# Performance work log

Hardware: AMD Instinct MI355X
Metric: run time of the kernel (lower is better)

## Reference

```python
import jax, jax.numpy as jnp
import numpy as np

N = 100000   # nodes / embedding vocab
E = 1600000  # edges
D = 128      # feature dim
R = 7        # num relations
B = 4096     # matches
EPS = 1e-5


def setup_inputs() -> dict:
    key = jax.random.key(0)
    ks = jax.random.split(key, 12)
    s = 0.05
    return {
        "x": jnp.arange(N, dtype=jnp.int32),
        "edge_index": jax.random.randint(ks[0], (2, E), 0, N, dtype=jnp.int32),
        "edge_type": jax.random.randint(ks[1], (E,), 0, R, dtype=jnp.int32),
        "home": jax.random.randint(ks[2], (B,), 0, N, dtype=jnp.int32),
        "away": jax.random.randint(ks[3], (B,), 0, N, dtype=jnp.int32),
        "embed": jax.random.normal(ks[4], (N, D), jnp.float32) * s,
        "rel_w": jax.random.normal(ks[5], (3, R, D, D), jnp.float32) * s,
        "root_w": jax.random.normal(ks[6], (3, D, D), jnp.float32) * s,
        "conv_b": jnp.zeros((3, D), jnp.float32),
        "bn_gamma": jnp.ones((2, D), jnp.float32),
        "bn_beta": jnp.zeros((2, D), jnp.float32),
        "bn_mean": jnp.zeros((2, D), jnp.float32),
        "bn_var": jnp.ones((2, D), jnp.float32),
        "fc0_w": jax.random.normal(ks[7], (256, 2 * D), jnp.float32) * s,
        "fc0_b": jnp.zeros((256,), jnp.float32),
        "fc1_w": jax.random.normal(ks[8], (128, 256), jnp.float32) * s,
        "fc1_b": jnp.zeros((128,), jnp.float32),
        "fc2_w": jax.random.normal(ks[9], (3, 128), jnp.float32) * s,
        "fc2_b": jnp.zeros((3,), jnp.float32),
    }


def rgcn_conv(h, rel_w, root_w, bias, src, dst, seg):
    # PyG RGCNConv with aggr='mean': per-relation mean of source features,
    # aggregate-then-transform (valid since the relation transform is linear).
    n = h.shape[0]
    agg = jax.ops.segment_sum(h[src], seg, num_segments=n * R)      # [N*R, Din]
    cnt = jax.ops.segment_sum(jnp.ones((src.shape[0],), h.dtype), seg,
                              num_segments=n * R)                   # [N*R]
    agg = (agg / jnp.maximum(cnt, 1.0)[:, None]).reshape(n, R, -1)  # [N, R, Din]
    return jnp.einsum('nri,rio->no', agg, rel_w) + h @ root_w + bias


def reference(x, edge_index, edge_type, home, away, embed, rel_w, root_w, conv_b,
              bn_gamma, bn_beta, bn_mean, bn_var,
              fc0_w, fc0_b, fc1_w, fc1_b, fc2_w, fc2_b):
    src, dst = edge_index[0], edge_index[1]
    seg = dst.astype(jnp.int32) * R + edge_type  # combined (node, relation) id

    h = embed[x]  # [N, D]
    for l in range(2):
        h = rgcn_conv(h, rel_w[l], root_w[l], conv_b[l], src, dst, seg)
        h = (h - bn_mean[l]) * jax.lax.rsqrt(bn_var[l] + EPS) * bn_gamma[l] + bn_beta[l]
        h = jax.nn.relu(h)
    h = rgcn_conv(h, rel_w[2], root_w[2], conv_b[2], src, dst, seg)

    g = jnp.concatenate([h[home], h[away]], axis=1)  # [B, 2D]
    g = jax.nn.relu(g @ fc0_w.T + fc0_b)
    g = jax.nn.relu(g @ fc1_w.T + fc1_b)
    g = g @ fc2_w.T + fc2_b
    return jax.nn.log_softmax(g, axis=1)
```

## Files before the change

### kernel.cpp

```cpp
#include <hip/hip_runtime.h>
#include <hip/hip_bf16.h>

#define RR 7
#define EPSBN 1e-5f

typedef __attribute__((ext_vector_type(8))) __bf16 bf16x8;
typedef __attribute__((ext_vector_type(4))) float f32x4;
typedef __attribute__((ext_vector_type(2))) float f32x2;

__device__ __forceinline__ float uhi2f(unsigned int u) {
    union { unsigned int i; float f; } c; c.i = u; return c.f;
}
__device__ __forceinline__ unsigned short f2b(float f) {
    union { float f; unsigned int i; } c; c.f = f;
    unsigned int x = c.i;
    return (unsigned short)((x + 0x7fffu + ((x >> 16) & 1u)) >> 16);
}

__global__ void hist_k(const int* __restrict__ dst, const int* __restrict__ et,
                       int* __restrict__ cnt, int ne) {
    int e = blockIdx.x * 256 + threadIdx.x;
    if (e < ne) atomicAdd(&cnt[dst[e] * RR + et[e]], 1);
}
__global__ void scan1_k(const int* __restrict__ cnt, int* __restrict__ bsum, int n) {
    __shared__ int sh[256];
    int base = blockIdx.x << 10;
    int s = 0;
    for (int i = threadIdx.x; i < 1024; i += 256) { int idx = base + i; if (idx < n) s += cnt[idx]; }
    sh[threadIdx.x] = s; __syncthreads();
    for (int off = 128; off > 0; off >>= 1) {
        if (threadIdx.x < off) sh[threadIdx.x] += sh[threadIdx.x + off];
        __syncthreads();
    }
    if (threadIdx.x == 0) bsum[blockIdx.x] = sh[0];
}
__global__ void scan2_k(int* __restrict__ bsum, int nb) {
    __shared__ int sh[256];
    int t = threadIdx.x;
    int v[4]; int loc = 0;
#pragma unroll
    for (int i = 0; i < 4; ++i) { int idx = t * 4 + i; v[i] = (idx < nb) ? bsum[idx] : 0; loc += v[i]; }
    sh[t] = loc; __syncthreads();
    for (int off = 1; off < 256; off <<= 1) {
        int x = (t >= off) ? sh[t - off] : 0;
        __syncthreads();
        sh[t] += x;
        __syncthreads();
    }
    int ex = (t > 0) ? sh[t - 1] : 0;
#pragma unroll
    for (int i = 0; i < 4; ++i) { int idx = t * 4 + i; if (idx < nb) { int vv = v[i]; bsum[idx] = ex; ex += vv; } }
}
__global__ void scan3_k(const int* __restrict__ cnt, const int* __restrict__ boff,
                        int* __restrict__ ptr, int* __restrict__ cursor, int n, int total) {
    __shared__ int sh[256];
    int t = threadIdx.x;
    int base = (blockIdx.x << 10) + (t << 2);
    int v[4]; int loc = 0;
#pragma unroll
    for (int i = 0; i < 4; ++i) { int idx = base + i; v[i] = (idx < n) ? cnt[idx] : 0; loc += v[i]; }
    sh[t] = loc; __syncthreads();
    for (int off = 1; off < 256; off <<= 1) {
        int x = (t >= off) ? sh[t - off] : 0;
        __syncthreads();
        sh[t] += x;
        __syncthreads();
    }
    int ex = boff[blockIdx.x] + ((t > 0) ? sh[t - 1] : 0);
#pragma unroll
    for (int i = 0; i < 4; ++i) {
        int idx = base + i;
        if (idx < n) { ptr[idx] = ex; cursor[idx] = ex; ex += v[i]; }
    }
    if (blockIdx.x == 0 && t == 0) ptr[n] = total;
}
__global__ void scatter_k(const int* __restrict__ src, const int* __restrict__ dst,
                          const int* __restrict__ et, int* __restrict__ cursor,
                          int* __restrict__ ssorted, int ne) {
    int e = blockIdx.x * 256 + threadIdx.x;
    if (e < ne) {
        int seg = dst[e] * RR + et[e];
        int pos = atomicAdd(&cursor[seg], 1);
        ssorted[pos] = src[e];
    }
}

__global__ __launch_bounds__(256) void prep_w_k(const float* __restrict__ rel_w,
                                                const float* __restrict__ root_w,
                                                unsigned short* __restrict__ wall) {
    __shared__ unsigned short T[128][130];
    int l = blockIdx.x >> 3, kb = blockIdx.x & 7;
    const float* src = (kb < RR) ? rel_w + ((size_t)(l * RR + kb) << 14)
                                 : root_w + ((size_t)l << 14);
    int t = threadIdx.x;
    for (int c = t; c < 4096; c += 256) {
        float4 f = *(const float4*)(src + (c << 2));
        int i = c >> 5, o = (c & 31) << 2;
        T[i][o] = f2b(f.x); T[i][o+1] = f2b(f.y); T[i][o+2] = f2b(f.z); T[i][o+3] = f2b(f.w);
    }
    __syncthreads();
    unsigned short* dst = wall + ((size_t)blockIdx.x << 14);
    for (int c = t; c < 2048; c += 256) {
        int frag = c >> 6;
        int lane = c & 63;
        int ks = frag >> 3, nt = frag & 7;
        int o = (nt << 4) + (lane & 15);
        int ib = (ks << 5) + ((lane >> 4) << 3);
        uint4 o4;
        o4.x = (unsigned)T[ib+0][o] | ((unsigned)T[ib+1][o] << 16);
        o4.y = (unsigned)T[ib+2][o] | ((unsigned)T[ib+3][o] << 16);
        o4.z = (unsigned)T[ib+4][o] | ((unsigned)T[ib+5][o] << 16);
        o4.w = (unsigned)T[ib+6][o] | ((unsigned)T[ib+7][o] << 16);
        *(uint4*)(dst + (c << 3)) = o4;
    }
}
__global__ void prep_h_k(const int* __restrict__ x, const float* __restrict__ embed,
                         unsigned short* __restrict__ h, int n) {
    int i = blockIdx.x * 256 + threadIdx.x;
    if (i >= n * 16) return;
    int node = i >> 4, c8 = (i & 15) << 3;
    const float* e = embed + ((size_t)x[node] << 7) + c8;
    float4 f0 = *(const float4*)e;
    float4 f1 = *(const float4*)(e + 4);
    uint4 o4;
    o4.x = (unsigned)f2b(f0.x) | ((unsigned)f2b(f0.y) << 16);
    o4.y = (unsigned)f2b(f0.z) | ((unsigned)f2b(f0.w) << 16);
    o4.z = (unsigned)f2b(f1.x) | ((unsigned)f2b(f1.y) << 16);
    o4.w = (unsigned)f2b(f1.z) | ((unsigned)f2b(f1.w) << 16);
    *(uint4*)(h + ((size_t)node << 7) + c8) = o4;
}
__global__ void prep_misc_k(const float* __restrict__ fc0w, const float* __restrict__ fc1w,
                            float* __restrict__ w0t, float* __restrict__ w1t,
                            const float* __restrict__ conv_b,
                            const float* __restrict__ bn_g, const float* __restrict__ bn_b,
                            const float* __restrict__ bn_m, const float* __restrict__ bn_v,
                            float* __restrict__ AB) {
    int b = blockIdx.x;
    if (b < 256) {
        int idx = (b << 8) + threadIdx.x;
        int o = idx & 255, i = idx >> 8;
        w0t[idx] = fc0w[o * 256 + i];
    } else if (b < 384) {
        int idx = ((b - 256) << 8) + threadIdx.x;
        int o = idx & 127, i = idx >> 7;
        w1t[idx] = fc1w[o * 256 + i];
    } else {
        for (int t = threadIdx.x; t < 384; t += 256) {
            int l = t >> 7, j = t & 127;
            float A = 1.f, Bv = conv_b[(l << 7) + j];
            if (l < 2) {
                float sc = bn_g[(l << 7) + j] * rsqrtf(bn_v[(l << 7) + j] + EPSBN);
                A = sc;
                Bv = Bv * sc + (bn_b[(l << 7) + j] - bn_m[(l << 7) + j] * sc);
            }
            AB[(l << 8) + j] = A;
            AB[(l << 8) + 128 + j] = Bv;
        }
    }
}

#define PAIRF(w) ((f32x2){uhi2f((w) << 16), uhi2f((w) & 0xffff0000u)})
#define ACCP(b, u) { av2[(b)+0] += PAIRF((u).x); av2[(b)+1] += PAIRF((u).y); \
                     av2[(b)+2] += PAIRF((u).z); av2[(b)+3] += PAIRF((u).w); }
#define GATH(s) { const unsigned short* hp = h_in + ((size_t)(s) << 7) + (quad << 3); \
                  uint4 u0 = *(const uint4*)(hp);       uint4 u1 = *(const uint4*)(hp + 32); \
                  uint4 u2 = *(const uint4*)(hp + 64);  uint4 u3 = *(const uint4*)(hp + 96); \
                  ACCP(0, u0); ACCP(4, u1); ACCP(8, u2); ACCP(12, u3); }

__global__ __launch_bounds__(256, 4) void layer_k(
    const unsigned short* __restrict__ h_in,
    unsigned short* __restrict__ h_out,
    const unsigned short* __restrict__ wfrag,
    const float* __restrict__ AB,
    const int* __restrict__ seg_ptr, const int* __restrict__ src_sorted,
    const int* __restrict__ list_a, const int* __restrict__ list_b, int listB,
    int nout, int bnrelu)
{
    const int tid  = threadIdx.x;
    const int wave = tid >> 6;
    const int lane = tid & 63;
    const int n16  = lane & 15;
    const int quad = lane >> 4;
    const int row0 = blockIdx.x << 6;
    const int gidx = row0 + (wave << 4) + n16;
    const bool valid = gidx < nout;
    int gnode = 0;
    if (valid) {
        gnode = list_a ? (gidx < listB ? list_a[gidx] : list_b[gidx - listB]) : gidx;
    }

    int p[8];
    {
        int b = valid ? gnode * RR : 0;
#pragma unroll
        for (int i = 0; i < 8; ++i) p[i] = seg_ptr[b + i];
    }

    f32x4 acc[8];
#pragma unroll
    for (int i = 0; i < 8; ++i) acc[i] = (f32x4){0.f, 0.f, 0.f, 0.f};

    int sv0, sv1, sv2, sv3;
    { int e0 = p[0]; sv0 = src_sorted[e0]; sv1 = src_sorted[e0+1];
      sv2 = src_sorted[e0+2]; sv3 = src_sorted[e0+3]; }

    const unsigned short* wl = wfrag + (lane << 3);

#pragma unroll
    for (int kb = 0; kb < 8; ++kb) {
        f32x2 av2[16];
#pragma unroll
        for (int i = 0; i < 16; ++i) av2[i] = (f32x2){0.f, 0.f};
        float scale = 1.f;
        int nv0 = 0, nv1 = 0, nv2 = 0, nv3 = 0;
        if (kb < RR) {
            if (kb < RR - 1) {
                int en = p[kb + 1];
                nv0 = src_sorted[en]; nv1 = src_sorted[en+1];
                nv2 = src_sorted[en+2]; nv3 = src_sorted[en+3];
            }
            if (valid) {
                int e0 = p[kb], e1 = p[kb + 1];
                int cnt = e1 - e0;
                if (cnt > 0) scale = __builtin_amdgcn_rcpf((float)cnt);
                if (cnt > 0) GATH(sv0);
                if (cnt > 1) GATH(sv1);
                if (cnt > 2) GATH(sv2);
                if (cnt > 3) GATH(sv3);
                for (int e = e0 + 4; e < e1; ++e) {
                    int s = src_sorted[e];
                    GATH(s);
                }
            }
        } else {
            if (valid) GATH(gnode);
        }
        uint4 au[4];
#pragma unroll
        for (int ks = 0; ks < 4; ++ks) {
            unsigned pw[4];
#pragma unroll
            for (int m = 0; m < 4; ++m) {
                f32x2 q = av2[(ks << 2) + m] * scale;
                __hip_bfloat162 b2 = __float22bfloat162_rn(make_float2(q.x, q.y));
                unsigned u; __builtin_memcpy(&u, &b2, 4);
                pw[m] = u;
            }
            au[ks].x = pw[0]; au[ks].y = pw[1]; au[ks].z = pw[2]; au[ks].w = pw[3];
        }
        const unsigned short* wk = wl + (kb << 14);
#pragma unroll
        for (int ks = 0; ks < 4; ++ks) {
            bf16x8 af;
            __builtin_memcpy(&af, &au[ks], 16);
#pragma unroll
            for (int nt = 0; nt < 8; ++nt) {
                bf16x8 bfr = *(const bf16x8*)(wk + (((ks << 3) + nt) << 9));
                acc[nt] = __builtin_amdgcn_mfma_f32_16x16x32_bf16(af, bfr, acc[nt], 0, 0, 0);
            }
        }
        sv0 = nv0; sv1 = nv1; sv2 = nv2; sv3 = nv3;
    }

#pragma unroll
    for (int nt = 0; nt < 8; ++nt) {
        int j = (nt << 4) + n16;
        float Aj = AB[j];
        float Bj = AB[128 + j];
#pragma unroll
        for (int r = 0; r < 4; ++r) {
            int orow = row0 + (wave << 4) + (quad << 2) + r;
            if (orow < nout) {
                float v = acc[nt][r] * Aj + Bj;
                if (bnrelu) v = fmaxf(v, 0.f);
                h_out[((size_t)orow << 7) + j] = f2b(v);
            }
        }
    }
}

__global__ __launch_bounds__(256) void mlp_k(
    const unsigned short* __restrict__ hC,
    const float* __restrict__ w0t, const float* __restrict__ bb0,
    const float* __restrict__ w1t, const float* __restrict__ bb1,
    const float* __restrict__ w2, const float* __restrict__ bb2,
    float* __restrict__ out, int Bn)
{
    __shared__ __attribute__((aligned(16))) float g0[16][256];
    __shared__ __attribute__((aligned(16))) float g1[16][256];
    __shared__ float lg[16][4];
    int t = threadIdx.x;
    {
        int row = t >> 4;
        int cseg = (t & 15) << 4;
        int gr = (blockIdx.x << 4) + row;
        int gc = (gr < Bn) ? gr : 0;
        const unsigned short* sp = (cseg < 128) ? (hC + ((size_t)gc << 7) + cseg)
                                                : (hC + ((size_t)(Bn + gc) << 7) + (cseg - 128));
#pragma unroll
        for (int c8 = 0; c8 < 2; ++c8) {
            uint4 v = *(const uint4*)(sp + (c8 << 3));
            int base = cseg + (c8 << 3);
            g0[row][base+0] = uhi2f(v.x << 16); g0[row][base+1] = uhi2f(v.x & 0xffff0000u);
            g0[row][base+2] = uhi2f(v.y << 16); g0[row][base+3] = uhi2f(v.y & 0xffff0000u);
            g0[row][base+4] = uhi2f(v.z << 16); g0[row][base+5] = uhi2f(v.z & 0xffff0000u);
            g0[row][base+6] = uhi2f(v.w << 16); g0[row][base+7] = uhi2f(v.w & 0xffff0000u);
        }
    }
    __syncthreads();
    {
        float acc[16];
#pragma unroll
        for (int r = 0; r < 16; ++r) acc[r] = 0.f;
#pragma unroll 4
        for (int i = 0; i < 256; ++i) {
            float w = w0t[(i << 8) + t];
#pragma unroll
            for (int r = 0; r < 16; ++r) acc[r] += w * g0[r][i];
        }
        float bb = bb0[t];
#pragma unroll
        for (int r = 0; r < 16; ++r) g1[r][t] = fmaxf(acc[r] + bb, 0.f);
    }
    __syncthreads();
    {
        int o = t & 127, rg = t >> 7;
        float acc[8];
#pragma unroll
        for (int r = 0; r < 8; ++r) acc[r] = 0.f;
#pragma unroll 4
        for (int i = 0; i < 256; ++i) {
            float w = w1t[(i << 7) + o];
#pragma unroll
            for (int r = 0; r < 8; ++r) acc[r] += w * g1[(rg << 3) + r][i];
        }
        float bb = bb1[o];
#pragma unroll
        for (int r = 0; r < 8; ++r) g0[(rg << 3) + r][o] = fmaxf(acc[r] + bb, 0.f);
    }
    __syncthreads();
    if (t < 48) {
        int row = t / 3, cls = t - row * 3;
        const float* wr = w2 + (cls << 7);
        float a = 0.f;
        for (int i = 0; i < 128; i += 4) {
            float4 w = *(const float4*)(wr + i);
            float4 g = *(const float4*)&g0[row][i];
            a += w.x * g.x + w.y * g.y + w.z * g.z + w.w * g.w;
        }
        lg[row][cls] = a + bb2[cls];
    }
    __syncthreads();
    if (t < 16) {
        int gr = (blockIdx.x << 4) + t;
        if (gr < Bn) {
            float l0 = lg[t][0], l1 = lg[t][1], l2 = lg[t][2];
            float m = fmaxf(l0, fmaxf(l1, l2));
            float lse = m + logf(expf(l0 - m) + expf(l1 - m) + expf(l2 - m));
            out[gr * 3 + 0] = l0 - lse;
            out[gr * 3 + 1] = l1 - lse;
            out[gr * 3 + 2] = l2 - lse;
        }
    }
}

extern "C" void kernel_launch(void* const* d_in, const int* in_sizes, int n_in,
                              void* d_out, int out_size, void* d_ws, size_t ws_size,
                              hipStream_t stream) {
    const int*   x      = (const int*)d_in[0];
    const int*   eidx   = (const int*)d_in[1];
    const int*   etype  = (const int*)d_in[2];
    const int*   home   = (const int*)d_in[3];
    const int*   away   = (const int*)d_in[4];
    const float* embed  = (const float*)d_in[5];
    const float* rel_w  = (const float*)d_in[6];
    const float* root_w = (const float*)d_in[7];
    const float* conv_b = (const float*)d_in[8];
    const float* bn_g   = (const float*)d_in[9];
    const float* bn_b   = (const float*)d_in[10];
    const float* bn_m   = (const float*)d_in[11];
    const float* bn_v   = (const float*)d_in[12];
    const float* fc0w   = (const float*)d_in[13];
    const float* fc0b   = (const float*)d_in[14];
    const float* fc1w   = (const float*)d_in[15];
    const float* fc1b   = (const float*)d_in[16];
    const float* fc2w   = (const float*)d_in[17];
    const float* fc2b   = (const float*)d_in[18];
    float* out = (float*)d_out;

    const int N_ = in_sizes[0];
    const int E_ = in_sizes[2];
    const int B_ = in_sizes[3];
    const int NS = N_ * RR;

    char* ws = (char*)d_ws;
    auto alloc = [&](size_t bytes) -> char* {
        char* p = ws;
        ws += (bytes + 255) & ~(size_t)255;
        return p;
    };
    int* ptr         = (int*)alloc((size_t)(NS + 1) * 4);
    int* cursor      = (int*)alloc((size_t)NS * 4);
    int* bsum        = (int*)alloc(4096);
    int* src_sorted  = (int*)alloc((size_t)(E_ + 16) * 4);
    unsigned short* wall = (unsigned short*)alloc((size_t)3 * 8 * 16384 * 2);
    unsigned short* hA   = (unsigned short*)alloc((size_t)N_ * 128 * 2);
    unsigned short* hB   = (unsigned short*)alloc((size_t)N_ * 128 * 2);
    unsigned short* hC   = (unsigned short*)alloc((size_t)2 * B_ * 128 * 2);
    float* AB        = (float*)alloc(3 * 256 * 4);
    float* w0t       = (float*)alloc(65536 * 4);
    float* w1t       = (float*)alloc(32768 * 4);

    const int nb = (NS + 1023) / 1024;

    (void)hipMemsetAsync(cursor, 0, (size_t)NS * 4, stream);
    hist_k<<<(E_ + 255) / 256, 256, 0, stream>>>(eidx + E_, etype, cursor, E_);
    scan1_k<<<nb, 256, 0, stream>>>(cursor, bsum, NS);
    scan2_k<<<1, 256, 0, stream>>>(bsum, nb);
    scan3_k<<<nb, 256, 0, stream>>>(cursor, bsum, ptr, cursor, NS, E_);
    scatter_k<<<(E_ + 255) / 256, 256, 0, stream>>>(eidx, eidx + E_, etype, cursor, src_sorted, E_);

    prep_w_k<<<24, 256, 0, stream>>>(rel_w, root_w, wall);
    prep_h_k<<<(N_ * 16 + 255) / 256, 256, 0, stream>>>(x, embed, hA, N_);
    prep_misc_k<<<385, 256, 0, stream>>>(fc0w, fc1w, w0t, w1t,
                                         conv_b, bn_g, bn_b, bn_m, bn_v, AB);

    const int lgrid = (N_ + 63) / 64;
    layer_k<<<lgrid, 256, 0, stream>>>(hA, hB, wall + 0 * 8 * 16384, AB + 0,
                                       ptr, src_sorted, nullptr, nullptr, 0, N_, 1);
    layer_k<<<lgrid, 256, 0, stream>>>(hB, hA, wall + 1 * 8 * 16384, AB + 256,
                                       ptr, src_sorted, nullptr, nullptr, 0, N_, 1);
    const int n3 = 2 * B_;
    layer_k<<<(n3 + 63) / 64, 256, 0, stream>>>(hA, hC, wall + 2 * 8 * 16384, AB + 512,
                                                ptr, src_sorted, home, away, B_, n3, 0);

    mlp_k<<<(B_ + 15) / 16, 256, 0, stream>>>(hC, w0t, fc0b, w1t, fc1b,
                                              fc2w, fc2b, out, B_);
}
```

Baseline: 682.0 us.

## Merge prep kernels and batch first four neighbor gathers before accumulation

Folds the three preprocessing kernels (weight fragment packing, embedding bf16 conversion, misc FC/BN prep) into one launch dispatched by block index, removing two kernel launches. In the layer kernel, the cross-relation software prefetch of source indices is replaced by issuing all four leading neighbor row loads up front into registers before accumulating, to raise memory-level parallelism. To fit the extra registers, launch bounds occupancy drops from 4 to 3 blocks per CU, which may reduce latency hiding. The prep kernel now carries a 33KB shared array even in blocks that never use it, which could limit how many of those blocks fit per CU.

```diff
diff --git a/kernel.cpp b/kernel.cpp
--- a/kernel.cpp
+++ b/kernel.cpp
@@ -85,68 +85,70 @@
     }
 }
 
-__global__ __launch_bounds__(256) void prep_w_k(const float* __restrict__ rel_w,
-                                                const float* __restrict__ root_w,
-                                                unsigned short* __restrict__ wall) {
+__global__ __launch_bounds__(256) void prep_all_k(
+    const float* __restrict__ rel_w, const float* __restrict__ root_w,
+    unsigned short* __restrict__ wall,
+    const int* __restrict__ x, const float* __restrict__ embed,
+    unsigned short* __restrict__ h, int n, int nhb,
+    const float* __restrict__ fc0w, const float* __restrict__ fc1w,
+    float* __restrict__ w0t, float* __restrict__ w1t,
+    const float* __restrict__ conv_b,
+    const float* __restrict__ bn_g, const float* __restrict__ bn_b,
+    const float* __restrict__ bn_m, const float* __restrict__ bn_v,
+    float* __restrict__ AB)
+{
     __shared__ unsigned short T[128][130];
-    int l = blockIdx.x >> 3, kb = blockIdx.x & 7;
-    const float* src = (kb < RR) ? rel_w + ((size_t)(l * RR + kb) << 14)
-                                 : root_w + ((size_t)l << 14);
+    int b = blockIdx.x;
     int t = threadIdx.x;
-    for (int c = t; c < 4096; c += 256) {
-        float4 f = *(const float4*)(src + (c << 2));
-        int i = c >> 5, o = (c & 31) << 2;
-        T[i][o] = f2b(f.x); T[i][o+1] = f2b(f.y); T[i][o+2] = f2b(f.z); T[i][o+3] = f2b(f.w);
-    }
-    __syncthreads();
-    unsigned short* dst = wall + ((size_t)blockIdx.x << 14);
-    for (int c = t; c < 2048; c += 256) {
-        int frag = c >> 6;
-        int lane = c & 63;
-        int ks = frag >> 3, nt = frag & 7;
-        int o = (nt << 4) + (lane & 15);
-        int ib = (ks << 5) + ((lane >> 4) << 3);
-        uint4 o4;
-        o4.x = (unsigned)T[ib+0][o] | ((unsigned)T[ib+1][o] << 16);
-        o4.y = (unsigned)T[ib+2][o] | ((unsigned)T[ib+3][o] << 16);
-        o4.z = (unsigned)T[ib+4][o] | ((unsigned)T[ib+5][o] << 16);
-        o4.w = (unsigned)T[ib+6][o] | ((unsigned)T[ib+7][o] << 16);
-        *(uint4*)(dst + (c << 3)) = o4;
-    }
-}
-__global__ void prep_h_k(const int* __restrict__ x, const float* __restrict__ embed,
-                         unsigned short* __restrict__ h, int n) {
-    int i = blockIdx.x * 256 + threadIdx.x;
-    if (i >= n * 16) return;
-    int node = i >> 4, c8 = (i & 15) << 3;
-    const float* e = embed + ((size_t)x[node] << 7) + c8;
-    float4 f0 = *(const float4*)e;
-    float4 f1 = *(const float4*)(e + 4);
-    uint4 o4;
-    o4.x = (unsigned)f2b(f0.x) | ((unsigned)f2b(f0.y) << 16);
-    o4.y = (unsigned)f2b(f0.z) | ((unsigned)f2b(f0.w) << 16);
-    o4.z = (unsigned)f2b(f1.x) | ((unsigned)f2b(f1.y) << 16);
-    o4.w = (unsigned)f2b(f1.z) | ((unsigned)f2b(f1.w) << 16);
-    *(uint4*)(h + ((size_t)node << 7) + c8) = o4;
-}
-__global__ void prep_misc_k(const float* __restrict__ fc0w, const float* __restrict__ fc1w,
-                            float* __restrict__ w0t, float* __restrict__ w1t,
-                            const float* __restrict__ conv_b,
-                            const float* __restrict__ bn_g, const float* __restrict__ bn_b,
-                            const float* __restrict__ bn_m, const float* __restrict__ bn_v,
-                            float* __restrict__ AB) {
-    int b = blockIdx.x;
-    if (b < 256) {
-        int idx = (b << 8) + threadIdx.x;
+    if (b < 24) {
+        int l = b >> 3, kb = b & 7;
+        const float* src = (kb < RR) ? rel_w + ((size_t)(l * RR + kb) << 14)
+                                     : root_w + ((size_t)l << 14);
+        for (int c = t; c < 4096; c += 256) {
+            float4 f = *(const float4*)(src + (c << 2));
+            int i = c >> 5, o = (c & 31) << 2;
+            T[i][o] = f2b(f.x); T[i][o+1] = f2b(f.y); T[i][o+2] = f2b(f.z); T[i][o+3] = f2b(f.w);
+        }
+        __syncthreads();
+        unsigned short* dst = wall + ((size_t)b << 14);
+        for (int c = t; c < 2048; c += 256) {
+            int frag = c >> 6;
+            int lane = c & 63;
+            int ks = frag >> 3, nt = frag & 7;
+            int o = (nt << 4) + (lane & 15);
+            int ib = (ks << 5) + ((lane >> 4) << 3);
+            uint4 o4;
+            o4.x = (unsigned)T[ib+0][o] | ((unsigned)T[ib+1][o] << 16);
+            o4.y = (unsigned)T[ib+2][o] | ((unsigned)T[ib+3][o] << 16);
+            o4.z = (unsigned)T[ib+4][o] | ((unsigned)T[ib+5][o] << 16);
+            o4.w = (unsigned)T[ib+6][o] | ((unsigned)T[ib+7][o] << 16);
+            *(uint4*)(dst + (c << 3)) = o4;
+        }
+    } else if (b < 24 + nhb) {
+        int i = (b - 24) * 256 + t;
+        if (i < n * 16) {
+            int node = i >> 4, c8 = (i & 15) << 3;
+            const float* e = embed + ((size_t)x[node] << 7) + c8;
+            float4 f0 = *(const float4*)e;
+            float4 f1 = *(const float4*)(e + 4);
+            uint4 o4;
+            o4.x = (unsigned)f2b(f0.x) | ((unsigned)f2b(f0.y) << 16);
+            o4.y = (unsigned)f2b(f0.z) | ((unsigned)f2b(f0.w) << 16);
+            o4.z = (unsigned)f2b(f1.x) | ((unsigned)f2b(f1.y) << 16);
+            o4.w = (unsigned)f2b(f1.z) | ((unsigned)f2b(f1.w) << 16);
+            *(uint4*)(h + ((size_t)node << 7) + c8) = o4;
+        }
+    } else if (b < 24 + nhb + 256) {
+        int idx = ((b - 24 - nhb) << 8) + t;
         int o = idx & 255, i = idx >> 8;
         w0t[idx] = fc0w[o * 256 + i];
-    } else if (b < 384) {
-        int idx = ((b - 256) << 8) + threadIdx.x;
+    } else if (b < 24 + nhb + 384) {
+        int idx = ((b - 24 - nhb - 256) << 8) + t;
         int o = idx & 127, i = idx >> 7;
         w1t[idx] = fc1w[o * 256 + i];
     } else {
-        for (int t = threadIdx.x; t < 384; t += 256) {
-            int l = t >> 7, j = t & 127;
+        for (int q = t; q < 384; q += 256) {
+            int l = q >> 7, j = q & 127;
             float A = 1.f, Bv = conv_b[(l << 7) + j];
             if (l < 2) {
                 float sc = bn_g[(l << 7) + j] * rsqrtf(bn_v[(l << 7) + j] + EPSBN);
@@ -166,8 +168,11 @@
                   uint4 u0 = *(const uint4*)(hp);       uint4 u1 = *(const uint4*)(hp + 32); \
                   uint4 u2 = *(const uint4*)(hp + 64);  uint4 u3 = *(const uint4*)(hp + 96); \
                   ACCP(0, u0); ACCP(4, u1); ACCP(8, u2); ACCP(12, u3); }
-
-__global__ __launch_bounds__(256, 4) void layer_k(
+#define LOAD4(dst, s) { const unsigned short* hp = h_in + ((size_t)(s) << 7) + (quad << 3); \
+                  (dst)[0] = *(const uint4*)(hp);      (dst)[1] = *(const uint4*)(hp + 32); \
+                  (dst)[2] = *(const uint4*)(hp + 64); (dst)[3] = *(const uint4*)(hp + 96); }
+
+__global__ __launch_bounds__(256, 3) void layer_k(
     const unsigned short* __restrict__ h_in,
     unsigned short* __restrict__ h_out,
     const unsigned short* __restrict__ wfrag,
@@ -200,10 +205,6 @@
 #pragma unroll
     for (int i = 0; i < 8; ++i) acc[i] = (f32x4){0.f, 0.f, 0.f, 0.f};
 
-    int sv0, sv1, sv2, sv3;
-    { int e0 = p[0]; sv0 = src_sorted[e0]; sv1 = src_sorted[e0+1];
-      sv2 = src_sorted[e0+2]; sv3 = src_sorted[e0+3]; }
-
     const unsigned short* wl = wfrag + (lane << 3);
 
 #pragma unroll
@@ -212,25 +213,26 @@
 #pragma unroll
         for (int i = 0; i < 16; ++i) av2[i] = (f32x2){0.f, 0.f};
         float scale = 1.f;
-        int nv0 = 0, nv1 = 0, nv2 = 0, nv3 = 0;
         if (kb < RR) {
-            if (kb < RR - 1) {
-                int en = p[kb + 1];
-                nv0 = src_sorted[en]; nv1 = src_sorted[en+1];
-                nv2 = src_sorted[en+2]; nv3 = src_sorted[en+3];
-            }
-            if (valid) {
-                int e0 = p[kb], e1 = p[kb + 1];
-                int cnt = e1 - e0;
-                if (cnt > 0) scale = __builtin_amdgcn_rcpf((float)cnt);
-                if (cnt > 0) GATH(sv0);
-                if (cnt > 1) GATH(sv1);
-                if (cnt > 2) GATH(sv2);
-                if (cnt > 3) GATH(sv3);
-                for (int e = e0 + 4; e < e1; ++e) {
-                    int s = src_sorted[e];
-                    GATH(s);
-                }
+            int e0 = p[kb], e1 = p[kb + 1];
+            int cnt = valid ? (e1 - e0) : 0;
+            if (cnt > 0) scale = __builtin_amdgcn_rcpf((float)cnt);
+            int s0 = src_sorted[e0];
+            int s1 = src_sorted[e0 + 1];
+            int s2 = src_sorted[e0 + 2];
+            int s3 = src_sorted[e0 + 3];
+            uint4 u[16];
+            if (cnt > 0) LOAD4(u + 0,  s0);
+            if (cnt > 1) LOAD4(u + 4,  s1);
+            if (cnt > 2) LOAD4(u + 8,  s2);
+            if (cnt > 3) LOAD4(u + 12, s3);
+            if (cnt > 0) { ACCP(0, u[0]);  ACCP(4, u[1]);  ACCP(8, u[2]);  ACCP(12, u[3]);  }
+            if (cnt > 1) { ACCP(0, u[4]);  ACCP(4, u[5]);  ACCP(8, u[6]);  ACCP(12, u[7]);  }
+            if (cnt > 2) { ACCP(0, u[8]);  ACCP(4, u[9]);  ACCP(8, u[10]); ACCP(12, u[11]); }
+            if (cnt > 3) { ACCP(0, u[12]); ACCP(4, u[13]); ACCP(8, u[14]); ACCP(12, u[15]); }
+            for (int e = e0 + 4; e < e0 + cnt; ++e) {
+                int s = src_sorted[e];
+                GATH(s);
             }
         } else {
             if (valid) GATH(gnode);
@@ -243,8 +245,8 @@
             for (int m = 0; m < 4; ++m) {
                 f32x2 q = av2[(ks << 2) + m] * scale;
                 __hip_bfloat162 b2 = __float22bfloat162_rn(make_float2(q.x, q.y));
-                unsigned u; __builtin_memcpy(&u, &b2, 4);
-                pw[m] = u;
+                unsigned uu; __builtin_memcpy(&uu, &b2, 4);
+                pw[m] = uu;
             }
             au[ks].x = pw[0]; au[ks].y = pw[1]; au[ks].z = pw[2]; au[ks].w = pw[3];
         }
@@ -259,7 +261,6 @@
                 acc[nt] = __builtin_amdgcn_mfma_f32_16x16x32_bf16(af, bfr, acc[nt], 0, 0, 0);
             }
         }
-        sv0 = nv0; sv1 = nv1; sv2 = nv2; sv3 = nv3;
     }
 
 #pragma unroll
@@ -412,6 +413,7 @@
     float* w1t       = (float*)alloc(32768 * 4);
 
     const int nb = (NS + 1023) / 1024;
+    const int nhb = (N_ * 16 + 255) / 256;
 
     (void)hipMemsetAsync(cursor, 0, (size_t)NS * 4, stream);
     hist_k<<<(E_ + 255) / 256, 256, 0, stream>>>(eidx + E_, etype, cursor, E_);
@@ -420,10 +422,9 @@
     scan3_k<<<nb, 256, 0, stream>>>(cursor, bsum, ptr, cursor, NS, E_);
     scatter_k<<<(E_ + 255) / 256, 256, 0, stream>>>(eidx, eidx + E_, etype, cursor, src_sorted, E_);
 
-    prep_w_k<<<24, 256, 0, stream>>>(rel_w, root_w, wall);
-    prep_h_k<<<(N_ * 16 + 255) / 256, 256, 0, stream>>>(x, embed, hA, N_);
-    prep_misc_k<<<385, 256, 0, stream>>>(fc0w, fc1w, w0t, w1t,
-                                         conv_b, bn_g, bn_b, bn_m, bn_v, AB);
+    prep_all_k<<<24 + nhb + 384 + 1, 256, 0, stream>>>(
+        rel_w, root_w, wall, x, embed, hA, N_, nhb,
+        fc0w, fc1w, w0t, w1t, conv_b, bn_g, bn_b, bn_m, bn_v, AB);
 
     const int lgrid = (N_ + 63) / 64;
     layer_k<<<lgrid, 256, 0, stream>>>(hA, hB, wall + 0 * 8 * 16384, AB + 0,
```

New measurement: 886.7 us. 30.0% more time.
